# Kernel tuning notes

Hardware: AMD Instinct MI355X
Metric: run time of the kernel (lower is better)

## Reference

```python
import jax, jax.numpy as jnp
import numpy as np

WS = 12        # window size (both q and k)
D_MODEL = 128
NHEAD = 8
HEAD_DIM = D_MODEL // NHEAD
SCALE = HEAD_DIM ** -0.5
EPS = 1e-5


def layernorm(x, g, b):
    m = jnp.mean(x, axis=-1, keepdims=True)
    v = jnp.mean(jnp.square(x - m), axis=-1, keepdims=True)
    return (x - m) * jax.lax.rsqrt(v + EPS) * g + b


def win_part(x, ws):
    # x: (B, H, W, C) -> (B * H/ws * W/ws, ws*ws, C)
    B, H, W, C = x.shape
    x = x.reshape(B, H // ws, ws, W // ws, ws, C)
    x = x.transpose(0, 1, 3, 2, 4, 5)
    return x.reshape(-1, ws * ws, C)


def resize_bilinear_ac(x, out_h, out_w):
    # NHWC bilinear with align_corners=True
    B, H, W, C = x.shape
    ys = jnp.linspace(0.0, H - 1.0, out_h)
    xs = jnp.linspace(0.0, W - 1.0, out_w)
    y0 = jnp.floor(ys).astype(jnp.int32)
    y1 = jnp.minimum(y0 + 1, H - 1)
    wy = (ys - y0)[None, :, None, None]
    x0 = jnp.floor(xs).astype(jnp.int32)
    x1 = jnp.minimum(x0 + 1, W - 1)
    wx = (xs - x0)[None, None, :, None]
    row = x[:, y0] * (1.0 - wy) + x[:, y1] * wy      # (B, out_h, W, C)
    return row[:, :, x0] * (1.0 - wx) + row[:, :, x1] * wx


def avgpool_ws(x_nchw, ws):
    # AvgPool2d(kernel=ws) with stride=ws, floor mode -> crop then mean
    B, C, H, W = x_nchw.shape
    Hc, Wc = (H // ws) * ws, (W // ws) * ws
    x = x_nchw[:, :, :Hc, :Wc].reshape(B, C, Hc // ws, ws, Wc // ws, ws)
    return x.mean(axis=(3, 5))  # (B, C, H//ws, W//ws)


def heads(x, B_, N):
    return x.reshape(B_, N, NHEAD, HEAD_DIM).transpose(0, 2, 1, 3)


def setup_inputs() -> dict:
    key = jax.random.key(0)
    ks = jax.random.split(key, 20)
    B, C1, C2, H, W = 4, 256, 128, 192, 192
    d, dh = D_MODEL, int(D_MODEL * 2)

    def lin(k, fin, fout):
        std = math_sqrt = (2.0 / (fin + fout)) ** 0.5
        return jax.random.normal(k, (fin, fout), jnp.float32) * std

    inp = {
        'x1': jax.random.normal(ks[0], (B, C1, H, W), jnp.float32),
        'x2': jax.random.normal(ks[1], (B, C2, H, W), jnp.float32),
        'Wq': lin(ks[2], C2, d), 'bq': jnp.zeros((d,), jnp.float32),
        'Wk': lin(ks[3], C1, d), 'bk': jnp.zeros((d,), jnp.float32),
        'Wv': lin(ks[4], C1, d), 'bv': jnp.zeros((d,), jnp.float32),
        'Wq2': lin(ks[5], C2, d), 'bq2': jnp.zeros((d,), jnp.float32),
        'Wk2': lin(ks[6], C1, d), 'bk2': jnp.zeros((d,), jnp.float32),
        'Wv2': lin(ks[7], C1, d), 'bv2': jnp.zeros((d,), jnp.float32),
        'Wproj': lin(ks[8], C1, d), 'bproj': jnp.zeros((d,), jnp.float32),
        'gproj': jnp.ones((d,), jnp.float32), 'bproj_ln': jnp.zeros((d,), jnp.float32),
        'g1': jnp.ones((d,), jnp.float32), 'b1': jnp.zeros((d,), jnp.float32),
        'Wfc1': lin(ks[9], d, dh), 'bfc1': jnp.zeros((dh,), jnp.float32),
        'Wfc2': lin(ks[10], dh, d), 'bfc2': jnp.zeros((d,), jnp.float32),
        'g2': jnp.ones((d,), jnp.float32), 'b2': jnp.zeros((d,), jnp.float32),
    }
    return inp


def reference(x1, x2, Wq, bq, Wk, bk, Wv, bv, Wq2, bq2, Wk2, bk2, Wv2, bv2,
              Wproj, bproj, gproj, bproj_ln, g1, b1, Wfc1, bfc1, Wfc2, bfc2, g2, b2):
    B, C1, H1, W1 = x1.shape
    _, C2, H2, W2 = x2.shape

    x1h = x1.transpose(0, 2, 3, 1)  # (B,H1,W1,C1)
    shortcut = jax.nn.gelu(layernorm(x1h @ Wproj + bproj, gproj, bproj_ln), approximate=False)
    shortcut = resize_bilinear_ac(shortcut, H2, W2)

    pad_b1 = (WS - H1 % WS) % WS
    pad_r1 = (WS - W1 % WS) % WS
    x1p = jnp.pad(x1h, ((0, 0), (0, pad_b1), (0, pad_r1), (0, 0)))
    H1p, W1p = x1p.shape[1], x1p.shape[2]

    x2h = x2.transpose(0, 2, 3, 1)
    pad_b2 = (WS - H2 % WS) % WS
    pad_r2 = (WS - W2 % WS) % WS
    x2p = jnp.pad(x2h, ((0, 0), (0, pad_b2), (0, pad_r2), (0, 0)))
    H2p, W2p = x2p.shape[1], x2p.shape[2]

    # ---- local windowed cross-attention (NOTE: no softmax, as in source) ----
    qw = win_part(x2p, WS)                 # (B_, N1, C2)
    kw = win_part(x1p, WS)                 # (B_, N2, C1)
    B_, N1, _ = qw.shape
    N2 = kw.shape[1]
    q = heads(qw @ Wq + bq, B_, N1) * SCALE     # (B_, h, N1, hd)
    k = heads(kw @ Wk + bk, B_, N2)
    v = heads(kw @ Wv + bv, B_, N2)
    attn = jnp.einsum('bhqd,bhkd->bhqk', q, k)
    ql = jnp.einsum('bhqk,bhkd->bhqd', attn, v)
    ql = ql.transpose(0, 2, 1, 3).reshape(B_, N1, D_MODEL)
    # merge windows back -> (B, H2p, W2p, d)
    ql = ql.reshape(B, H2p // WS, W2p // WS, WS, WS, D_MODEL)
    ql = ql.transpose(0, 1, 3, 2, 4, 5).reshape(B, H2p, W2p, D_MODEL)

    # ---- global pooled cross-attention (with softmax) ----
    qg = avgpool_ws(x2, WS).transpose(0, 2, 3, 1).reshape(B, -1, C2)   # (B, nW, C2)
    kg = avgpool_ws(x1, WS).transpose(0, 2, 3, 1).reshape(B, -1, C1)   # (B, nW, C1)
    nW = qg.shape[1]
    qg_ = heads(qg @ Wq2 + bq2, B, nW) * SCALE
    kg_ = heads(kg @ Wk2 + bk2, B, nW)
    vg_ = heads(kg @ Wv2 + bv2, B, nW)
    a = jax.nn.softmax(jnp.einsum('bhqd,bhkd->bhqk', qg_, kg_), axis=-1)
    qgo = jnp.einsum('bhqk,bhkd->bhqd', a, vg_).transpose(0, 2, 1, 3).reshape(B, nW, D_MODEL)
    qgo = qgo.reshape(B, H2p // WS, W2p // WS, D_MODEL)
    qgo = resize_bilinear_ac(qgo, H2p, W2p)

    q_sum = ql + qgo
    q_sum = q_sum[:, :H2, :W2, :]

    h = layernorm(q_sum, g1, b1)
    h = jax.nn.gelu(h @ Wfc1 + bfc1, approximate=False) @ Wfc2 + bfc2  # Mlp (dropout=eval)
    out = layernorm(shortcut + h, g2, b2)
    return out.transpose(0, 3, 1, 2)  # (B, d_model, H2, W2)
```

## Files before the change

### kernel.cpp

```cpp
#include <hip/hip_runtime.h>


typedef unsigned short u16;
typedef unsigned int   u32;
typedef __bf16 bf16x8 __attribute__((ext_vector_type(8)));
typedef float  f32x4  __attribute__((ext_vector_type(4)));

__device__ __forceinline__ float b2f(u16 x) {
    union { u32 u; float f; } v; v.u = ((u32)x) << 16; return v.f;
}
__device__ __forceinline__ u16 f2b(float f) {
    union { float f; u32 u; } v; v.f = f;
    return (u16)((v.u + 0x7fffu + ((v.u >> 16) & 1u)) >> 16);
}
__device__ __forceinline__ u32 cvtpk(float lo, float hi) {
    u32 r;
    asm("v_cvt_pk_bf16_f32 %0, %1, %2" : "=v"(r) : "v"(lo), "v"(hi));
    return r;
}
__device__ __forceinline__ float gelu_fast(float x) {
    float z = x * 0.70710678118654752f;
    float a = fabsf(z);
    float t = __builtin_amdgcn_rcpf(fmaf(0.3275911f, a, 1.0f));
    float p = t*(0.254829592f + t*(-0.284496736f + t*(1.421413741f
              + t*(-1.453152027f + t*1.061405429f))));
    float e = __expf(-a*a);
    float er = copysignf(fmaf(-p, e, 1.0f), z);
    return 0.5f * x * (1.0f + er);
}
__device__ __forceinline__ void unpack8(uint4 r, float* v) {
    v[0] = b2f((u16)(r.x & 0xffff)); v[1] = b2f((u16)(r.x >> 16));
    v[2] = b2f((u16)(r.y & 0xffff)); v[3] = b2f((u16)(r.y >> 16));
    v[4] = b2f((u16)(r.z & 0xffff)); v[5] = b2f((u16)(r.z >> 16));
    v[6] = b2f((u16)(r.w & 0xffff)); v[7] = b2f((u16)(r.w >> 16));
}
__device__ __forceinline__ uint4 pack8(const float* v) {
    uint4 r;
    r.x = cvtpk(v[0], v[1]);
    r.y = cvtpk(v[2], v[3]);
    r.z = cvtpk(v[4], v[5]);
    r.w = cvtpk(v[6], v[7]);
    return r;
}

__launch_bounds__(256)
__global__ void setup_weights(const float* Wq, const float* Wk, const float* Wv,
    const float* Wq2, const float* Wk2, const float* Wv2, const float* Wproj,
    const float* Wfc1, const float* Wfc2, const float* bk, const float* bv,
    const float* bk2, const float* bv2,
    u16* wt_proj, u16* wt_kv, u16* wt_q, u16* wt_fc1, u16* wt_fc2,
    u16* wt_q2, u16* wt_k2v2, float* bkv, float* bk2v2)
{
    long i = (long)blockIdx.x*256 + threadIdx.x;
    if (i < 32768) { int k=(int)(i>>7), n=(int)(i&127); wt_proj[n*256+k]=f2b(Wproj[i]); return; } i -= 32768;
    if (i < 32768) { int k=(int)(i>>7), n=(int)(i&127); wt_kv[n*256+k]=f2b(Wk[i]); return; } i -= 32768;
    if (i < 32768) { int k=(int)(i>>7), n=(int)(i&127); wt_kv[(128+n)*256+k]=f2b(Wv[i]); return; } i -= 32768;
    if (i < 16384) { int k=(int)(i>>7), n=(int)(i&127); wt_q[n*128+k]=f2b(Wq[i]); return; } i -= 16384;
    if (i < 32768) { int k=(int)(i>>8), n=(int)(i&255); wt_fc1[n*128+k]=f2b(Wfc1[i]); return; } i -= 32768;
    if (i < 32768) { int k=(int)(i>>7), n=(int)(i&127); wt_fc2[n*256+k]=f2b(Wfc2[i]); return; } i -= 32768;
    if (i < 16384) { int k=(int)(i>>7), n=(int)(i&127); wt_q2[n*128+k]=f2b(Wq2[i]); return; } i -= 16384;
    if (i < 32768) { int k=(int)(i>>7), n=(int)(i&127); wt_k2v2[n*256+k]=f2b(Wk2[i]); return; } i -= 32768;
    if (i < 32768) { int k=(int)(i>>7), n=(int)(i&127); wt_k2v2[(128+n)*256+k]=f2b(Wv2[i]); return; } i -= 32768;
    if (i < 128) { bkv[i]=bk[i]; return; } i -= 128;
    if (i < 128) { bkv[128+i]=bv[i]; return; } i -= 128;
    if (i < 128) { bk2v2[i]=bk2[i]; return; } i -= 128;
    if (i < 128) { bk2v2[128+i]=bv2[i]; return; }
}

__launch_bounds__(256)
__global__ void proj_kv(const float* __restrict__ Af,
                        const u16* __restrict__ WtP, const float* __restrict__ biasP,
                        const float* __restrict__ gw, const float* __restrict__ bw,
                        const u16* __restrict__ WtKV, const float* __restrict__ biasKV,
                        u16* __restrict__ outSC, u16* __restrict__ outKV)
{
    constexpr int KD = 256, AST = KD + 8;
    __shared__ alignas(16) u16 a_sm[64*AST];
    __shared__ float pls[256], plq[256];
    const int t = threadIdx.x, w = t>>6, lane = t&63, lrow = lane&15, quad = lane>>4;

    const long row0 = (long)blockIdx.x*64;
    {
        const int bb = (int)(row0/36864); const long p0 = row0 % 36864;
        const int c0 = (t>>3)*2, pj = (t&7)*8;
#pragma unroll
        for (int cc = 0; cc < 4; cc++) {
            int c = c0 + cc*64;
            const float* s0 = Af + ((long)bb*KD + c)*36864 + p0 + pj;
            const float* s1 = s0 + 36864;
            float4 a0 = *(const float4*)s0, a1 = *(const float4*)(s0+4);
            float4 b0 = *(const float4*)s1, b1 = *(const float4*)(s1+4);
            *(u32*)&a_sm[(pj+0)*AST + c] = cvtpk(a0.x, b0.x);
            *(u32*)&a_sm[(pj+1)*AST + c] = cvtpk(a0.y, b0.y);
            *(u32*)&a_sm[(pj+2)*AST + c] = cvtpk(a0.z, b0.z);
            *(u32*)&a_sm[(pj+3)*AST + c] = cvtpk(a0.w, b0.w);
            *(u32*)&a_sm[(pj+4)*AST + c] = cvtpk(a1.x, b1.x);
            *(u32*)&a_sm[(pj+5)*AST + c] = cvtpk(a1.y, b1.y);
            *(u32*)&a_sm[(pj+6)*AST + c] = cvtpk(a1.z, b1.z);
            *(u32*)&a_sm[(pj+7)*AST + c] = cvtpk(a1.w, b1.w);
        }
    }
    __builtin_amdgcn_sched_barrier(0);

    bf16x8 WBp[2][8];
    float bcolp[2], gcol[2], bwcol[2];
#pragma unroll
    for (int n = 0; n < 2; n++) {
        int col = w*32 + n*16 + lrow;
#pragma unroll
        for (int k = 0; k < 8; k++)
            WBp[n][k] = *(const bf16x8*)&WtP[(size_t)col*KD + k*32 + quad*8];
        bcolp[n] = biasP[col]; gcol[n] = gw[col]; bwcol[n] = bw[col];
    }
    __syncthreads();

    f32x4 acc[4][2];
#pragma unroll
    for (int rt = 0; rt < 4; rt++)
#pragma unroll
        for (int n = 0; n < 2; n++) { f32x4 z = {0.f,0.f,0.f,0.f}; acc[rt][n] = z; }
#pragma unroll
    for (int rt = 0; rt < 4; rt++) {
        bf16x8 af[8];
#pragma unroll
        for (int k = 0; k < 8; k++)
            af[k] = *(const bf16x8*)&a_sm[(rt*16+lrow)*AST + k*32 + quad*8];
#pragma unroll
        for (int n = 0; n < 2; n++)
#pragma unroll
            for (int k = 0; k < 8; k++)
                acc[rt][n] = __builtin_amdgcn_mfma_f32_16x16x32_bf16(af[k], WBp[n][k], acc[rt][n], 0, 0, 0);
    }
    __builtin_amdgcn_sched_barrier(0);

#pragma unroll
    for (int rt = 0; rt < 4; rt++)
#pragma unroll
        for (int r = 0; r < 4; r++) {
            float s = 0.f, sq = 0.f;
#pragma unroll
            for (int n = 0; n < 2; n++) {
                float v = acc[rt][n][r] + bcolp[n];
                acc[rt][n][r] = v; s += v; sq += v*v;
            }
#pragma unroll
            for (int off = 1; off < 16; off <<= 1) { s += __shfl_xor(s, off); sq += __shfl_xor(sq, off); }
            if (lrow == 0) { int ri = rt*16 + quad*4 + r; pls[w*64+ri] = s; plq[w*64+ri] = sq; }
        }

    bf16x8 WBk[2][8];
    float bcolk[2];
#pragma unroll
    for (int n = 0; n < 2; n++) {
        int col = w*64 + n*16 + lrow;
#pragma unroll
        for (int k = 0; k < 8; k++)
            WBk[n][k] = *(const bf16x8*)&WtKV[(size_t)col*KD + k*32 + quad*8];
        bcolk[n] = biasKV[col];
    }
    __syncthreads();

#pragma unroll
    for (int rt = 0; rt < 4; rt++)
#pragma unroll
        for (int r = 0; r < 4; r++) {
            int ri = rt*16 + quad*4 + r;
            float s  = pls[ri] + pls[64+ri] + pls[128+ri] + pls[192+ri];
            float sq = plq[ri] + plq[64+ri] + plq[128+ri] + plq[192+ri];
            float mean = s*(1.0f/128.0f);
            float var = sq*(1.0f/128.0f) - mean*mean;
            float rstd = rsqrtf(var + 1e-5f);
            float y0 = (acc[rt][0][r]-mean)*rstd*gcol[0] + bwcol[0];
            float y1 = (acc[rt][1][r]-mean)*rstd*gcol[1] + bwcol[1];
            u32 pr = cvtpk(gelu_fast(y0), gelu_fast(y1));
            long o = (row0+ri)*128 + w*32 + lrow;
            outSC[o]      = (u16)pr;
            outSC[o + 16] = (u16)(pr >> 16);
        }
    __builtin_amdgcn_sched_barrier(0);

#pragma unroll
    for (int rt = 0; rt < 4; rt++) {
        bf16x8 af[8];
#pragma unroll
        for (int k = 0; k < 8; k++)
            af[k] = *(const bf16x8*)&a_sm[(rt*16+lrow)*AST + k*32 + quad*8];
        f32x4 a2[2];
#pragma unroll
        for (int n = 0; n < 2; n++) { f32x4 z = {0.f,0.f,0.f,0.f}; a2[n] = z; }
#pragma unroll
        for (int n = 0; n < 2; n++)
#pragma unroll
            for (int k = 0; k < 8; k++)
                a2[n] = __builtin_amdgcn_mfma_f32_16x16x32_bf16(af[k], WBk[n][k], a2[n], 0, 0, 0);
#pragma unroll
        for (int r = 0; r < 4; r++) {
            u32 pr = cvtpk(a2[0][r] + bcolk[0], a2[1][r] + bcolk[1]);
            long o = (row0 + rt*16 + quad*4 + r)*256 + w*64 + lrow;
            outKV[o]      = (u16)pr;
            outKV[o + 16] = (u16)(pr >> 16);
        }
    }
    __builtin_amdgcn_sched_barrier(0);

#pragma unroll
    for (int n = 0; n < 2; n++) {
        int col = w*64 + 32 + n*16 + lrow;
#pragma unroll
        for (int k = 0; k < 8; k++)
            WBk[n][k] = *(const bf16x8*)&WtKV[(size_t)col*KD + k*32 + quad*8];
        bcolk[n] = biasKV[col];
    }
#pragma unroll
    for (int rt = 0; rt < 4; rt++) {
        bf16x8 af[8];
#pragma unroll
        for (int k = 0; k < 8; k++)
            af[k] = *(const bf16x8*)&a_sm[(rt*16+lrow)*AST + k*32 + quad*8];
        f32x4 a2[2];
#pragma unroll
        for (int n = 0; n < 2; n++) { f32x4 z = {0.f,0.f,0.f,0.f}; a2[n] = z; }
#pragma unroll
        for (int n = 0; n < 2; n++)
#pragma unroll
            for (int k = 0; k < 8; k++)
                a2[n] = __builtin_amdgcn_mfma_f32_16x16x32_bf16(af[k], WBk[n][k], a2[n], 0, 0, 0);
#pragma unroll
        for (int r = 0; r < 4; r++) {
            u32 pr = cvtpk(a2[0][r] + bcolk[0], a2[1][r] + bcolk[1]);
            long o = (row0 + rt*16 + quad*4 + r)*256 + w*64 + 32 + lrow;
            outKV[o]      = (u16)pr;
            outKV[o + 16] = (u16)(pr >> 16);
        }
    }
}

template<int KD, int ND, int EPI, int NCHW_IN>
__launch_bounds__(256)
__global__ void gemm_rw(const float* __restrict__ Af, const u16* __restrict__ Ab,
                        const u16* __restrict__ Wt, const float* __restrict__ bias,
                        u16* __restrict__ out, float scale, int nTiles)
{
    constexpr int KS = KD/32, NW = ND/4, NT = NW/16, AST = KD + 8;
    __shared__ alignas(16) u16 a_sm[64*AST];
    const int t = threadIdx.x, w = t>>6, lane = t&63, lrow = lane&15, quad = lane>>4;

    bf16x8 WB[NT][KS];
    float bcol[NT];
#pragma unroll
    for (int n = 0; n < NT; n++) {
        int col = w*NW + n*16 + lrow;
#pragma unroll
        for (int k = 0; k < KS; k++)
            WB[n][k] = *(const bf16x8*)&Wt[(size_t)col*KD + k*32 + quad*8];
        bcol[n] = bias[col];
    }

    for (int tile = blockIdx.x; tile < nTiles; tile += gridDim.x) {
        const long row0 = (long)tile*64;
        __syncthreads();
        if (NCHW_IN) {
            const int bb = (int)(row0/36864); const long p0 = row0 % 36864;
            const int c0 = (t>>3)*2, pj = (t&7)*8;
#pragma unroll
            for (int cc = 0; cc < KD/64; cc++) {
                int c = c0 + cc*64;
                const float* s0 = Af + ((long)bb*KD + c)*36864 + p0 + pj;
                const float* s1 = s0 + 36864;
                float4 a0 = *(const float4*)s0, a1 = *(const float4*)(s0+4);
                float4 b0 = *(const float4*)s1, b1 = *(const float4*)(s1+4);
                *(u32*)&a_sm[(pj+0)*AST + c] = cvtpk(a0.x, b0.x);
                *(u32*)&a_sm[(pj+1)*AST + c] = cvtpk(a0.y, b0.y);
                *(u32*)&a_sm[(pj+2)*AST + c] = cvtpk(a0.z, b0.z);
                *(u32*)&a_sm[(pj+3)*AST + c] = cvtpk(a0.w, b0.w);
                *(u32*)&a_sm[(pj+4)*AST + c] = cvtpk(a1.x, b1.x);
                *(u32*)&a_sm[(pj+5)*AST + c] = cvtpk(a1.y, b1.y);
                *(u32*)&a_sm[(pj+6)*AST + c] = cvtpk(a1.z, b1.z);
                *(u32*)&a_sm[(pj+7)*AST + c] = cvtpk(a1.w, b1.w);
            }
        } else {
            const int am = t>>2, ak = (t&3)*(KD/4);
#pragma unroll
            for (int j = 0; j < KD/32; j++)
                *(uint4*)&a_sm[am*AST + ak + j*8] = *(const uint4*)&Ab[(row0+am)*KD + ak + j*8];
        }
        __syncthreads();

#pragma unroll
        for (int rt = 0; rt < 4; rt++) {
            bf16x8 af[KS];
#pragma unroll
            for (int k = 0; k < KS; k++)
                af[k] = *(const bf16x8*)&a_sm[(rt*16+lrow)*AST + k*32 + quad*8];
            f32x4 acc[NT];
#pragma unroll
            for (int n = 0; n < NT; n++) { f32x4 z = {0.f,0.f,0.f,0.f}; acc[n] = z; }
#pragma unroll
            for (int n = 0; n < NT; n++)
#pragma unroll
                for (int k = 0; k < KS; k++)
                    acc[n] = __builtin_amdgcn_mfma_f32_16x16x32_bf16(af[k], WB[n][k], acc[n], 0, 0, 0);
#pragma unroll
            for (int n = 0; n < NT; n++) {
                int col = w*NW + n*16 + lrow;
#pragma unroll
                for (int r = 0; r < 4; r++)
                    out[(row0 + rt*16 + quad*4 + r)*ND + col] = f2b((acc[n][r] + bcol[n]) * scale);
            }
        }
    }
}

template<int C>
__launch_bounds__(256)
__global__ void avgpool_nchw(const float* __restrict__ X, u16* __restrict__ out)
{
    int blk = blockIdx.x;
    int bb = blk / C, c = blk % C;
    int t = threadIdx.x;
    int wy = t >> 4, wx = t & 15;
    const float* base = X + ((long)(bb*C + c))*36864;
    float s = 0.f;
    for (int py = 0; py < 12; py++) {
        long ro = (long)(wy*12+py)*192 + wx*12;
#pragma unroll
        for (int px = 0; px < 12; px++) s += base[ro + px];
    }
    out[((long)(bb*256 + t))*C + c] = f2b(s * (1.0f/144.0f));
}

__launch_bounds__(256)
__global__ void global_attn(const u16* __restrict__ qg, const u16* __restrict__ kv,
                            float* __restrict__ qgo)
{
    int t = threadIdx.x;
    int wvq = t >> 6, lane = t & 63;
    int bid = blockIdx.x;
    int qb = bid & 63, bh = bid >> 6;
    int bb = bh >> 3, h = bh & 7;
    int q = qb*4 + wvq;

    const u16* qrow = qg + ((long)(bb*256 + q))*128 + h*16;
    float qv[16];
#pragma unroll
    for (int d = 0; d < 16; d++) qv[d] = b2f(qrow[d]);

    float s[4];
#pragma unroll
    for (int jj = 0; jj < 4; jj++) {
        int j = jj*64 + lane;
        const u16* krow = kv + ((long)(bb*256 + j))*256 + h*16;
        float a = 0.f;
#pragma unroll
        for (int d = 0; d < 16; d++) a += qv[d] * b2f(krow[d]);
        s[jj] = a;
    }
    float m = fmaxf(fmaxf(s[0], s[1]), fmaxf(s[2], s[3]));
#pragma unroll
    for (int off = 1; off < 64; off <<= 1) m = fmaxf(m, __shfl_xor(m, off));
    float p[4]; float lsum = 0.f;
#pragma unroll
    for (int jj = 0; jj < 4; jj++) { p[jj] = expf(s[jj] - m); lsum += p[jj]; }
#pragma unroll
    for (int off = 1; off < 64; off <<= 1) lsum += __shfl_xor(lsum, off);

    float acc[16];
#pragma unroll
    for (int d = 0; d < 16; d++) acc[d] = 0.f;
#pragma unroll
    for (int jj = 0; jj < 4; jj++) {
        int j = jj*64 + lane;
        const u16* vrow = kv + ((long)(bb*256 + j))*256 + 128 + h*16;
#pragma unroll
        for (int d = 0; d < 16; d++) acc[d] += p[jj] * b2f(vrow[d]);
    }
#pragma unroll
    for (int d = 0; d < 16; d++) {
        float x = acc[d];
#pragma unroll
        for (int off = 1; off < 64; off <<= 1) x += __shfl_xor(x, off);
        acc[d] = x;
    }
    if (lane == 0) {
        float inv = 1.0f / lsum;
        float* dst = qgo + ((long)(bb*256 + q))*128 + h*16;
#pragma unroll
        for (int d = 0; d < 16; d++) dst[d] = acc[d] * inv;
    }
}

__launch_bounds__(256)
__global__ void window_kv(const u16* __restrict__ KV, float* __restrict__ KVw)
{
    __shared__ alignas(16) u16 kvs[72*256];
    int t = threadIdx.x;
    int wid = blockIdx.x;
    int bb = wid >> 8, wy = (wid >> 4) & 15, wx = wid & 15;
    int h = t >> 5, rem = t & 31, ii = rem >> 1, j0 = (rem & 1)*8;
    float acc[8];
#pragma unroll
    for (int j = 0; j < 8; j++) acc[j] = 0.f;

    for (int chunk = 0; chunk < 2; chunk++) {
        __syncthreads();
        for (int pass = 0; pass < 5; pass++) {
            int nn = pass*16 + (t >> 4);
            if (nn < 72) {
                int n = chunk*72 + nn;
                int py = n/12, px = n%12;
                long row = (long)bb*36864 + (long)(wy*12+py)*192 + wx*12+px;
                int ch = (t & 15)*16;
                *(uint4*)&kvs[nn*256 + ch]     = *(const uint4*)&KV[row*256 + ch];
                *(uint4*)&kvs[nn*256 + ch + 8] = *(const uint4*)&KV[row*256 + ch + 8];
            }
        }
        __syncthreads();
        for (int nn = 0; nn < 72; nn++) {
            float kvv = b2f(kvs[nn*256 + h*16 + ii]);
            uint4 vr = *(const uint4*)&kvs[nn*256 + 128 + h*16 + j0];
            float vv[8]; unpack8(vr, vv);
#pragma unroll
            for (int j = 0; j < 8; j++) acc[j] += kvv * vv[j];
        }
    }
    float* dst = KVw + (((long)wid*8 + h)*16 + ii)*16 + j0;
#pragma unroll
    for (int j = 0; j < 8; j++) dst[j] = acc[j];
}

__launch_bounds__(256)
__global__ void window_out(const u16* __restrict__ Q, const float* __restrict__ KVw,
                           const float* __restrict__ qgo, const float* __restrict__ gw,
                           const float* __restrict__ bw, u16* __restrict__ Hout)
{
    __shared__ alignas(16) u16 qs[144*136];
    __shared__ alignas(16) float kvs[8*264];
    int t = threadIdx.x;
    int wid = blockIdx.x;
    int bb = wid >> 8, wy = (wid >> 4) & 15, wx = wid & 15;

    for (int pass = 0; pass < 9; pass++) {
        int n = pass*16 + (t >> 4);
        int py = n/12, px = n%12;
        long row = (long)bb*36864 + (long)(wy*12+py)*192 + wx*12+px;
        int ch = (t & 15)*8;
        *(uint4*)&qs[n*136 + ch] = *(const uint4*)&Q[row*128 + ch];
    }
    {
        const float* src = KVw + (long)wid*2048;
        for (int e = t; e < 2048; e += 256) {
            int hh = e >> 8, rem2 = e & 255;
            kvs[hh*264 + rem2] = src[e];
        }
    }
    __syncthreads();
    int td = t & 15;
    int h = td & 7, j0 = (td >> 3)*8;
    int cbase = h*16 + j0;
    float gv8[8], bv8[8];
#pragma unroll
    for (int j = 0; j < 8; j++) { gv8[j] = gw[cbase+j]; bv8[j] = bw[cbase+j]; }

    for (int pass = 0; pass < 9; pass++) {
        int pi = pass*16 + (t >> 4);
        int py = pi/12, px = pi%12;
        int y = wy*12+py, x = wx*12+px;
        float acc[8];
#pragma unroll
        for (int j = 0; j < 8; j++) acc[j] = 0.f;
#pragma unroll
        for (int i = 0; i < 16; i++) {
            float qv = b2f(qs[pi*136 + h*16 + i]);
            const float* kp = &kvs[h*264 + i*16 + j0];
            float4 ka = *(const float4*)kp;
            float4 kb = *(const float4*)(kp + 4);
            acc[0] += qv*ka.x; acc[1] += qv*ka.y; acc[2] += qv*ka.z; acc[3] += qv*ka.w;
            acc[4] += qv*kb.x; acc[5] += qv*kb.y; acc[6] += qv*kb.z; acc[7] += qv*kb.w;
        }
        float syf = y * (15.0f/191.0f);
        int y0 = (int)syf; float fy = syf - y0; int y1 = min(y0+1, 15);
        float sxf = x * (15.0f/191.0f);
        int x0 = (int)sxf; float fx = sxf - x0; int x1 = min(x0+1, 15);
        const float* g00 = qgo + (((long)bb*16 + y0)*16 + x0)*128 + cbase;
        const float* g01 = qgo + (((long)bb*16 + y0)*16 + x1)*128 + cbase;
        const float* g10 = qgo + (((long)bb*16 + y1)*16 + x0)*128 + cbase;
        const float* g11 = qgo + (((long)bb*16 + y1)*16 + x1)*128 + cbase;
        float w00 = (1.f-fy)*(1.f-fx), w01 = (1.f-fy)*fx, w10 = fy*(1.f-fx), w11 = fy*fx;
        float v8[8];
        float sum = 0.f, sq = 0.f;
#pragma unroll
        for (int j = 0; j < 8; j++) {
            float gval = w00*g00[j] + w01*g01[j] + w10*g10[j] + w11*g11[j];
            float xv = acc[j] + gval;
            v8[j] = xv; sum += xv; sq += xv*xv;
        }
#pragma unroll
        for (int off = 1; off < 16; off <<= 1) { sum += __shfl_xor(sum, off); sq += __shfl_xor(sq, off); }
        float mean = sum * (1.0f/128.0f);
        float var = sq * (1.0f/128.0f) - mean*mean;
        float rstd = rsqrtf(var + 1e-5f);
        float o8[8];
#pragma unroll
        for (int j = 0; j < 8; j++) o8[j] = (v8[j]-mean)*rstd*gv8[j] + bv8[j];
        long orow = (long)bb*36864 + (long)y*192 + x;
        *(uint4*)&Hout[orow*128 + cbase] = pack8(o8);
    }
}

__launch_bounds__(256)
__global__ void mlp_fused(const u16* __restrict__ H, const u16* __restrict__ W1t,
                          const float* __restrict__ b1f, const u16* __restrict__ W2t,
                          const float* __restrict__ b2f32, const u16* __restrict__ SC,
                          const float* __restrict__ g2, const float* __restrict__ bt2,
                          float* __restrict__ out, int nTiles)
{
    __shared__ alignas(16) char sm[53248];
    u16* h_sm  = (u16*)sm;
    u16* t_sm  = (u16*)(sm + 17408);
    float* pls = (float*)(sm + 51200);
    float* plq = (float*)(sm + 52224);
    float* lt  = (float*)sm;

    const int t = threadIdx.x, w = t>>6, lane = t&63, lrow = lane&15, quad = lane>>4;

    const long row0 = (long)blockIdx.x*64;
    const int bb = (int)(row0/36864); const long p0 = row0 % 36864;

    float scv[4][4][2];
#pragma unroll
    for (int rt = 0; rt < 4; rt++)
#pragma unroll
        for (int r = 0; r < 4; r++)
#pragma unroll
            for (int n = 0; n < 2; n++)
                scv[rt][r][n] = b2f(SC[(row0 + rt*16 + quad*4 + r)*128 + w*32 + n*16 + lrow]);

    bf16x8 WB1[4][4];
    float b1col[4];
#pragma unroll
    for (int n = 0; n < 4; n++) {
        int col = w*64 + n*16 + lrow;
#pragma unroll
        for (int k = 0; k < 4; k++)
            WB1[n][k] = *(const bf16x8*)&W1t[(size_t)col*128 + k*32 + quad*8];
        b1col[n] = b1f[col];
    }

    {
        const int am = t>>2, ak = (t&3)*32;
#pragma unroll
        for (int j = 0; j < 4; j++)
            *(uint4*)&h_sm[am*136 + ak + j*8] = *(const uint4*)&H[(row0+am)*128 + ak + j*8];
    }
    __syncthreads();

#pragma unroll
    for (int rt = 0; rt < 4; rt++) {
        bf16x8 af[4];
#pragma unroll
        for (int k = 0; k < 4; k++)
            af[k] = *(const bf16x8*)&h_sm[(rt*16+lrow)*136 + k*32 + quad*8];
        f32x4 a1[4];
#pragma unroll
        for (int n = 0; n < 4; n++) { f32x4 z = {0.f,0.f,0.f,0.f}; a1[n] = z; }
#pragma unroll
        for (int n = 0; n < 4; n++)
#pragma unroll
            for (int k = 0; k < 4; k++)
                a1[n] = __builtin_amdgcn_mfma_f32_16x16x32_bf16(af[k], WB1[n][k], a1[n], 0, 0, 0);
#pragma unroll
        for (int n = 0; n < 4; n++)
#pragma unroll
            for (int r = 0; r < 4; r++)
                t_sm[(rt*16+quad*4+r)*264 + w*64 + n*16 + lrow] = f2b(gelu_fast(a1[n][r] + b1col[n]));
    }
    __syncthreads();
    __builtin_amdgcn_sched_barrier(0);

    bf16x8 WB2[2][8];
    float b2col[2], gcol[2], bwcol[2];
#pragma unroll
    for (int n = 0; n < 2; n++) {
        int col = w*32 + n*16 + lrow;
#pragma unroll
        for (int k = 0; k < 8; k++)
            WB2[n][k] = *(const bf16x8*)&W2t[(size_t)col*256 + k*32 + quad*8];
        b2col[n] = b2f32[col]; gcol[n] = g2[col]; bwcol[n] = bt2[col];
    }

    f32x4 a2[4][2];
#pragma unroll
    for (int rt = 0; rt < 4; rt++)
#pragma unroll
        for (int n = 0; n < 2; n++) { f32x4 z = {0.f,0.f,0.f,0.f}; a2[rt][n] = z; }
#pragma unroll
    for (int rt = 0; rt < 4; rt++) {
        {
            bf16x8 af[4];
#pragma unroll
            for (int k = 0; k < 4; k++)
                af[k] = *(const bf16x8*)&t_sm[(rt*16+lrow)*264 + k*32 + quad*8];
#pragma unroll
            for (int n = 0; n < 2; n++)
#pragma unroll
                for (int k = 0; k < 4; k++)
                    a2[rt][n] = __builtin_amdgcn_mfma_f32_16x16x32_bf16(af[k], WB2[n][k], a2[rt][n], 0, 0, 0);
        }
        {
            bf16x8 af[4];
#pragma unroll
            for (int k = 0; k < 4; k++)
                af[k] = *(const bf16x8*)&t_sm[(rt*16+lrow)*264 + (k+4)*32 + quad*8];
#pragma unroll
            for (int n = 0; n < 2; n++)
#pragma unroll
                for (int k = 0; k < 4; k++)
                    a2[rt][n] = __builtin_amdgcn_mfma_f32_16x16x32_bf16(af[k], WB2[n][k+4], a2[rt][n], 0, 0, 0);
        }
    }

#pragma unroll
    for (int rt = 0; rt < 4; rt++)
#pragma unroll
        for (int r = 0; r < 4; r++) {
            float s = 0.f, sq = 0.f;
#pragma unroll
            for (int n = 0; n < 2; n++) {
                float v = a2[rt][n][r] + b2col[n] + scv[rt][r][n];
                a2[rt][n][r] = v; s += v; sq += v*v;
            }
#pragma unroll
            for (int off = 1; off < 16; off <<= 1) { s += __shfl_xor(s, off); sq += __shfl_xor(sq, off); }
            if (lrow == 0) { int ri = rt*16 + quad*4 + r; pls[w*64+ri] = s; plq[w*64+ri] = sq; }
        }
    __syncthreads();
#pragma unroll
    for (int rt = 0; rt < 4; rt++)
#pragma unroll
        for (int r = 0; r < 4; r++) {
            int ri = rt*16 + quad*4 + r;
            float s  = pls[ri] + pls[64+ri] + pls[128+ri] + pls[192+ri];
            float sq = plq[ri] + plq[64+ri] + plq[128+ri] + plq[192+ri];
            float mean = s*(1.0f/128.0f);
            float var = sq*(1.0f/128.0f) - mean*mean;
            float rstd = rsqrtf(var + 1e-5f);
#pragma unroll
            for (int n = 0; n < 2; n++)
                lt[(w*32 + n*16 + lrow)*68 + ri] = (a2[rt][n][r]-mean)*rstd*gcol[n] + bwcol[n];
        }
    __syncthreads();
    {
        const int cch = t>>1, ph = (t&1)*32;
        const float4* sp = (const float4*)&lt[cch*68 + ph];
        float4* dp = (float4*)&out[((long)(bb*128 + cch))*36864 + p0 + ph];
#pragma unroll
        for (int q2 = 0; q2 < 8; q2++) dp[q2] = sp[q2];
    }
}

extern "C" void kernel_launch(void* const* d_in, const int* in_sizes, int n_in,
                              void* d_out, int out_size, void* d_ws, size_t ws_size,
                              hipStream_t stream)
{
    const float* x1     = (const float*)d_in[0];
    const float* x2     = (const float*)d_in[1];
    const float* Wq     = (const float*)d_in[2];
    const float* bq     = (const float*)d_in[3];
    const float* Wk     = (const float*)d_in[4];
    const float* bk     = (const float*)d_in[5];
    const float* Wv     = (const float*)d_in[6];
    const float* bv     = (const float*)d_in[7];
    const float* Wq2    = (const float*)d_in[8];
    const float* bq2    = (const float*)d_in[9];
    const float* Wk2    = (const float*)d_in[10];
    const float* bk2    = (const float*)d_in[11];
    const float* Wv2    = (const float*)d_in[12];
    const float* bv2    = (const float*)d_in[13];
    const float* Wproj  = (const float*)d_in[14];
    const float* bproj  = (const float*)d_in[15];
    const float* gproj  = (const float*)d_in[16];
    const float* bprojln= (const float*)d_in[17];
    const float* g1     = (const float*)d_in[18];
    const float* b1     = (const float*)d_in[19];
    const float* Wfc1   = (const float*)d_in[20];
    const float* bfc1   = (const float*)d_in[21];
    const float* Wfc2   = (const float*)d_in[22];
    const float* bfc2   = (const float*)d_in[23];
    const float* g2     = (const float*)d_in[24];
    const float* b2v    = (const float*)d_in[25];

    char* ws = (char*)d_ws;
    u16*  WTPROJ = (u16*)(ws + 0L);
    u16*  WTKV   = (u16*)(ws + 65536L);
    u16*  WTQ    = (u16*)(ws + 196608L);
    u16*  WTFC1  = (u16*)(ws + 229376L);
    u16*  WTFC2  = (u16*)(ws + 294912L);
    u16*  WTQ2   = (u16*)(ws + 360448L);
    u16*  WTK2V2 = (u16*)(ws + 393216L);
    float* BKVf  = (float*)(ws + 524288L);
    float* BK2V2f= (float*)(ws + 525312L);
    u16*  KG     = (u16*)(ws + 1048576L);
    u16*  QG     = (u16*)(ws + 1572864L);
    u16*  QG2    = (u16*)(ws + 1835008L);
    u16*  KV2    = (u16*)(ws + 2097152L);
    float* QGO   = (float*)(ws + 2621440L);
    float* KVW   = (float*)(ws + 3145728L);
    u16*  REGA   = (u16*)(ws + 12582912L);
    u16*  SC     = (u16*)(ws + 88080384L);
    u16*  Q_H    = REGA;

    setup_weights<<<1026, 256, 0, stream>>>(Wq, Wk, Wv, Wq2, Wk2, Wv2, Wproj, Wfc1, Wfc2,
                                            bk, bv, bk2, bv2,
                                            WTPROJ, WTKV, WTQ, WTFC1, WTFC2, WTQ2, WTK2V2,
                                            BKVf, BK2V2f);
    proj_kv<<<2304, 256, 0, stream>>>(x1, WTPROJ, bproj, gproj, bprojln,
                                      WTKV, BKVf, SC, REGA);
    avgpool_nchw<256><<<1024, 256, 0, stream>>>(x1, KG);
    avgpool_nchw<128><<<512, 256, 0, stream>>>(x2, QG);
    gemm_rw<128,128,0,0><<<16, 256, 0, stream>>>(nullptr, QG, WTQ2, bq2, QG2, 0.25f, 16);
    gemm_rw<256,256,0,0><<<16, 256, 0, stream>>>(nullptr, KG, WTK2V2, BK2V2f, KV2, 1.0f, 16);
    global_attn<<<2048, 256, 0, stream>>>(QG2, KV2, QGO);
    window_kv<<<1024, 256, 0, stream>>>(REGA, KVW);
    gemm_rw<128,128,0,1><<<1152, 256, 0, stream>>>(x2, nullptr, WTQ, bq, Q_H, 0.25f, 2304);
    window_out<<<1024, 256, 0, stream>>>(Q_H, KVW, QGO, g1, b1, Q_H);
    mlp_fused<<<2304, 256, 0, stream>>>(Q_H, WTFC1, bfc1, WTFC2, bfc2, SC, g2, b2v, (float*)d_out, 2304);
}
```

Before: 621.0 us.

## Fuse window KV reduction, Q projection and window output into one kernel

Merges the window_kv, NCHW Q-projection GEMM and window_out kernels into a single per-window kernel. Each block computes its K^T V summary in shared memory, loads its own x2 window from NCHW, projects Q with MFMA, and applies the linear attention plus layernorm in place. The output is written into the K half of the interleaved KV buffer (stride 256), and the MLP reads it with that stride. This removes the KVW and Q_H round trips through global memory and two launches. In exchange, the per-window x2 loads use scalar 16-bit shared stores, and each block does more serial work.

```diff
diff --git a/kernel.cpp b/kernel.cpp
--- a/kernel.cpp
+++ b/kernel.cpp
@@ -235,9 +235,9 @@
     }
 }
 
-template<int KD, int ND, int EPI, int NCHW_IN>
+template<int KD, int ND>
 __launch_bounds__(256)
-__global__ void gemm_rw(const float* __restrict__ Af, const u16* __restrict__ Ab,
+__global__ void gemm_rw(const u16* __restrict__ Ab,
                         const u16* __restrict__ Wt, const float* __restrict__ bias,
                         u16* __restrict__ out, float scale, int nTiles)
 {
@@ -259,26 +259,7 @@
     for (int tile = blockIdx.x; tile < nTiles; tile += gridDim.x) {
         const long row0 = (long)tile*64;
         __syncthreads();
-        if (NCHW_IN) {
-            const int bb = (int)(row0/36864); const long p0 = row0 % 36864;
-            const int c0 = (t>>3)*2, pj = (t&7)*8;
-#pragma unroll
-            for (int cc = 0; cc < KD/64; cc++) {
-                int c = c0 + cc*64;
-                const float* s0 = Af + ((long)bb*KD + c)*36864 + p0 + pj;
-                const float* s1 = s0 + 36864;
-                float4 a0 = *(const float4*)s0, a1 = *(const float4*)(s0+4);
-                float4 b0 = *(const float4*)s1, b1 = *(const float4*)(s1+4);
-                *(u32*)&a_sm[(pj+0)*AST + c] = cvtpk(a0.x, b0.x);
-                *(u32*)&a_sm[(pj+1)*AST + c] = cvtpk(a0.y, b0.y);
-                *(u32*)&a_sm[(pj+2)*AST + c] = cvtpk(a0.z, b0.z);
-                *(u32*)&a_sm[(pj+3)*AST + c] = cvtpk(a0.w, b0.w);
-                *(u32*)&a_sm[(pj+4)*AST + c] = cvtpk(a1.x, b1.x);
-                *(u32*)&a_sm[(pj+5)*AST + c] = cvtpk(a1.y, b1.y);
-                *(u32*)&a_sm[(pj+6)*AST + c] = cvtpk(a1.z, b1.z);
-                *(u32*)&a_sm[(pj+7)*AST + c] = cvtpk(a1.w, b1.w);
-            }
-        } else {
+        {
             const int am = t>>2, ak = (t&3)*(KD/4);
 #pragma unroll
             for (int j = 0; j < KD/32; j++)
@@ -390,73 +371,112 @@
 }
 
 __launch_bounds__(256)
-__global__ void window_kv(const u16* __restrict__ KV, float* __restrict__ KVw)
+__global__ void window_fused(const u16* KV, const float* __restrict__ X2,
+                             const u16* __restrict__ WtQ, const float* __restrict__ bqv,
+                             const float* __restrict__ qgo, const float* __restrict__ gw,
+                             const float* __restrict__ bw, u16* Hout)
 {
-    __shared__ alignas(16) u16 kvs[72*256];
-    int t = threadIdx.x;
-    int wid = blockIdx.x;
-    int bb = wid >> 8, wy = (wid >> 4) & 15, wx = wid & 15;
-    int h = t >> 5, rem = t & 31, ii = rem >> 1, j0 = (rem & 1)*8;
-    float acc[8];
-#pragma unroll
-    for (int j = 0; j < 8; j++) acc[j] = 0.f;
-
-    for (int chunk = 0; chunk < 2; chunk++) {
+    __shared__ alignas(16) char sm[47616];
+    u16* kvs = (u16*)sm;
+    u16* xs  = (u16*)sm;
+    float* kvw = (float*)(sm + 39168);
+
+    const int t = threadIdx.x, w = t>>6, lane = t&63, lrow = lane&15, quad = lane>>4;
+    const int wid = blockIdx.x;
+    const int bb = wid >> 8, wy = (wid >> 4) & 15, wx = wid & 15;
+
+    {
+        int h = t >> 5, rem = t & 31, ii = rem >> 1, j0 = (rem & 1)*8;
+        float acc8[8];
+#pragma unroll
+        for (int j = 0; j < 8; j++) acc8[j] = 0.f;
+        for (int chunk = 0; chunk < 2; chunk++) {
+            __syncthreads();
+            for (int pass = 0; pass < 5; pass++) {
+                int nn = pass*16 + (t >> 4);
+                if (nn < 72) {
+                    int n = chunk*72 + nn;
+                    int py = n/12, px = n%12;
+                    long row = (long)bb*36864 + (long)(wy*12+py)*192 + wx*12+px;
+                    int ch = (t & 15)*16;
+                    *(uint4*)&kvs[nn*256 + ch]     = *(const uint4*)&KV[row*256 + ch];
+                    *(uint4*)&kvs[nn*256 + ch + 8] = *(const uint4*)&KV[row*256 + ch + 8];
+                }
+            }
+            __syncthreads();
+            for (int nn = 0; nn < 72; nn++) {
+                float kvv = b2f(kvs[nn*256 + h*16 + ii]);
+                uint4 vr = *(const uint4*)&kvs[nn*256 + 128 + h*16 + j0];
+                float vv[8]; unpack8(vr, vv);
+#pragma unroll
+                for (int j = 0; j < 8; j++) acc8[j] += kvv * vv[j];
+            }
+        }
+#pragma unroll
+        for (int j = 0; j < 8; j++) kvw[h*264 + ii*16 + j0 + j] = acc8[j];
+    }
+
+    bf16x8 WBq[2][4];
+    float bqc[2];
+#pragma unroll
+    for (int n = 0; n < 2; n++) {
+        int col = w*32 + n*16 + lrow;
+#pragma unroll
+        for (int k = 0; k < 4; k++)
+            WBq[n][k] = *(const bf16x8*)&WtQ[(size_t)col*128 + k*32 + quad*8];
+        bqc[n] = bqv[col];
+    }
+    __syncthreads();
+
+#pragma unroll
+    for (int i = 0; i < 6; i++) {
+        int p = t + 256*i;
+        int c = p & 127, py = p >> 7;
+        const float* src = X2 + ((long)bb*128 + c)*36864 + (long)(wy*12+py)*192 + wx*12;
+        float4 v0 = *(const float4*)src;
+        float4 v1 = *(const float4*)(src+4);
+        float4 v2 = *(const float4*)(src+8);
+        int rb = (py*12)*136 + c;
+        xs[rb +  0*136] = (u16)cvtpk(v0.x, v0.x);
+        xs[rb +  1*136] = (u16)cvtpk(v0.y, v0.y);
+        xs[rb +  2*136] = (u16)cvtpk(v0.z, v0.z);
+        xs[rb +  3*136] = (u16)cvtpk(v0.w, v0.w);
+        xs[rb +  4*136] = (u16)cvtpk(v1.x, v1.x);
+        xs[rb +  5*136] = (u16)cvtpk(v1.y, v1.y);
+        xs[rb +  6*136] = (u16)cvtpk(v1.z, v1.z);
+        xs[rb +  7*136] = (u16)cvtpk(v1.w, v1.w);
+        xs[rb +  8*136] = (u16)cvtpk(v2.x, v2.x);
+        xs[rb +  9*136] = (u16)cvtpk(v2.y, v2.y);
+        xs[rb + 10*136] = (u16)cvtpk(v2.z, v2.z);
+        xs[rb + 11*136] = (u16)cvtpk(v2.w, v2.w);
+    }
+    __syncthreads();
+
+    for (int s = 0; s < 9; s++) {
+        bf16x8 af[4];
+#pragma unroll
+        for (int k = 0; k < 4; k++)
+            af[k] = *(const bf16x8*)&xs[(s*16+lrow)*136 + k*32 + quad*8];
         __syncthreads();
-        for (int pass = 0; pass < 5; pass++) {
-            int nn = pass*16 + (t >> 4);
-            if (nn < 72) {
-                int n = chunk*72 + nn;
-                int py = n/12, px = n%12;
-                long row = (long)bb*36864 + (long)(wy*12+py)*192 + wx*12+px;
-                int ch = (t & 15)*16;
-                *(uint4*)&kvs[nn*256 + ch]     = *(const uint4*)&KV[row*256 + ch];
-                *(uint4*)&kvs[nn*256 + ch + 8] = *(const uint4*)&KV[row*256 + ch + 8];
-            }
-        }
-        __syncthreads();
-        for (int nn = 0; nn < 72; nn++) {
-            float kvv = b2f(kvs[nn*256 + h*16 + ii]);
-            uint4 vr = *(const uint4*)&kvs[nn*256 + 128 + h*16 + j0];
-            float vv[8]; unpack8(vr, vv);
-#pragma unroll
-            for (int j = 0; j < 8; j++) acc[j] += kvv * vv[j];
-        }
-    }
-    float* dst = KVw + (((long)wid*8 + h)*16 + ii)*16 + j0;
-#pragma unroll
-    for (int j = 0; j < 8; j++) dst[j] = acc[j];
-}
-
-__launch_bounds__(256)
-__global__ void window_out(const u16* __restrict__ Q, const float* __restrict__ KVw,
-                           const float* __restrict__ qgo, const float* __restrict__ gw,
-                           const float* __restrict__ bw, u16* __restrict__ Hout)
-{
-    __shared__ alignas(16) u16 qs[144*136];
-    __shared__ alignas(16) float kvs[8*264];
-    int t = threadIdx.x;
-    int wid = blockIdx.x;
-    int bb = wid >> 8, wy = (wid >> 4) & 15, wx = wid & 15;
-
-    for (int pass = 0; pass < 9; pass++) {
-        int n = pass*16 + (t >> 4);
-        int py = n/12, px = n%12;
-        long row = (long)bb*36864 + (long)(wy*12+py)*192 + wx*12+px;
-        int ch = (t & 15)*8;
-        *(uint4*)&qs[n*136 + ch] = *(const uint4*)&Q[row*128 + ch];
-    }
-    {
-        const float* src = KVw + (long)wid*2048;
-        for (int e = t; e < 2048; e += 256) {
-            int hh = e >> 8, rem2 = e & 255;
-            kvs[hh*264 + rem2] = src[e];
-        }
-    }
-    __syncthreads();
+        f32x4 aq[2];
+#pragma unroll
+        for (int n = 0; n < 2; n++) { f32x4 z = {0.f,0.f,0.f,0.f}; aq[n] = z; }
+#pragma unroll
+        for (int n = 0; n < 2; n++)
+#pragma unroll
+            for (int k = 0; k < 4; k++)
+                aq[n] = __builtin_amdgcn_mfma_f32_16x16x32_bf16(af[k], WBq[n][k], aq[n], 0, 0, 0);
+#pragma unroll
+        for (int n = 0; n < 2; n++)
+#pragma unroll
+            for (int r = 0; r < 4; r++)
+                xs[(s*16 + quad*4 + r)*136 + w*32 + n*16 + lrow] = f2b((aq[n][r] + bqc[n]) * 0.25f);
+    }
+    __syncthreads();
+
     int td = t & 15;
-    int h = td & 7, j0 = (td >> 3)*8;
-    int cbase = h*16 + j0;
+    int h2 = td & 7, j0c = (td >> 3)*8;
+    int cbase = h2*16 + j0c;
     float gv8[8], bv8[8];
 #pragma unroll
     for (int j = 0; j < 8; j++) { gv8[j] = gw[cbase+j]; bv8[j] = bw[cbase+j]; }
@@ -470,8 +490,8 @@
         for (int j = 0; j < 8; j++) acc[j] = 0.f;
 #pragma unroll
         for (int i = 0; i < 16; i++) {
-            float qv = b2f(qs[pi*136 + h*16 + i]);
-            const float* kp = &kvs[h*264 + i*16 + j0];
+            float qv = b2f(xs[pi*136 + h2*16 + i]);
+            const float* kp = &kvw[h2*264 + i*16 + j0c];
             float4 ka = *(const float4*)kp;
             float4 kb = *(const float4*)(kp + 4);
             acc[0] += qv*ka.x; acc[1] += qv*ka.y; acc[2] += qv*ka.z; acc[3] += qv*ka.w;
@@ -503,7 +523,7 @@
 #pragma unroll
         for (int j = 0; j < 8; j++) o8[j] = (v8[j]-mean)*rstd*gv8[j] + bv8[j];
         long orow = (long)bb*36864 + (long)y*192 + x;
-        *(uint4*)&Hout[orow*128 + cbase] = pack8(o8);
+        *(uint4*)&Hout[orow*256 + cbase] = pack8(o8);
     }
 }
 
@@ -550,7 +570,7 @@
         const int am = t>>2, ak = (t&3)*32;
 #pragma unroll
         for (int j = 0; j < 4; j++)
-            *(uint4*)&h_sm[am*136 + ak + j*8] = *(const uint4*)&H[(row0+am)*128 + ak + j*8];
+            *(uint4*)&h_sm[am*136 + ak + j*8] = *(const uint4*)&H[(row0+am)*256 + ak + j*8];
     }
     __syncthreads();
 
@@ -704,10 +724,8 @@
     u16*  QG2    = (u16*)(ws + 1835008L);
     u16*  KV2    = (u16*)(ws + 2097152L);
     float* QGO   = (float*)(ws + 2621440L);
-    float* KVW   = (float*)(ws + 3145728L);
     u16*  REGA   = (u16*)(ws + 12582912L);
     u16*  SC     = (u16*)(ws + 88080384L);
-    u16*  Q_H    = REGA;
 
     setup_weights<<<1026, 256, 0, stream>>>(Wq, Wk, Wv, Wq2, Wk2, Wv2, Wproj, Wfc1, Wfc2,
                                             bk, bv, bk2, bv2,
@@ -717,11 +735,9 @@
                                       WTKV, BKVf, SC, REGA);
     avgpool_nchw<256><<<1024, 256, 0, stream>>>(x1, KG);
     avgpool_nchw<128><<<512, 256, 0, stream>>>(x2, QG);
-    gemm_rw<128,128,0,0><<<16, 256, 0, stream>>>(nullptr, QG, WTQ2, bq2, QG2, 0.25f, 16);
-    gemm_rw<256,256,0,0><<<16, 256, 0, stream>>>(nullptr, KG, WTK2V2, BK2V2f, KV2, 1.0f, 16);
+    gemm_rw<128,128><<<16, 256, 0, stream>>>(QG, WTQ2, bq2, QG2, 0.25f, 16);
+    gemm_rw<256,256><<<16, 256, 0, stream>>>(KG, WTK2V2, BK2V2f, KV2, 1.0f, 16);
     global_attn<<<2048, 256, 0, stream>>>(QG2, KV2, QGO);
-    window_kv<<<1024, 256, 0, stream>>>(REGA, KVW);
-    gemm_rw<128,128,0,1><<<1152, 256, 0, stream>>>(x2, nullptr, WTQ, bq, Q_H, 0.25f, 2304);
-    window_out<<<1024, 256, 0, stream>>>(Q_H, KVW, QGO, g1, b1, Q_H);
-    mlp_fused<<<2304, 256, 0, stream>>>(Q_H, WTFC1, bfc1, WTFC2, bfc2, SC, g2, b2v, (float*)d_out, 2304);
-}
+    window_fused<<<1024, 256, 0, stream>>>(REGA, x2, WTQ, bq, QGO, g1, b1, REGA);
+    mlp_fused<<<2304, 256, 0, stream>>>(REGA, WTFC1, bfc1, WTFC2, bfc2, SC, g2, b2v, (float*)d_out, 2304);
+}
```

Measured after the change: 619.9 us. Within noise of the previous version (-0.2%).
